# Kernel tuning notes

Measured on AMD Instinct MI355X. Metric: run time of the kernel, lower is better.

Reference implementation:

```python
import jax, jax.numpy as jnp
import numpy as np

NUM_HEADS = 8
CUTOFF = 10.0


def layer_norm(x, g, b):
    m = x.mean(-1, keepdims=True)
    v = x.var(-1, keepdims=True)
    return (x - m) * jax.lax.rsqrt(v + 1e-5) * g + b


def mha(h, mask, Wq, Wk, Wv, Wo):
    # masked multi-head self-attention over the edge set; mask: [E,E] bool
    E, D = h.shape
    hd = D // NUM_HEADS
    q = (h @ Wq).reshape(E, NUM_HEADS, hd)
    k = (h @ Wk).reshape(E, NUM_HEADS, hd)
    v = (h @ Wv).reshape(E, NUM_HEADS, hd)
    s = jnp.einsum('ihd,jhd->hij', q, k) / jnp.sqrt(jnp.asarray(hd, h.dtype))
    s = jnp.where(mask[None], s, jnp.asarray(-1e9, h.dtype))
    p = jax.nn.softmax(s, axis=-1)  # [H,E,E]
    out = jnp.einsum('hij,jhd->ihd', p, v).reshape(E, D)
    return out @ Wo, p.mean(0)


def setup_inputs() -> dict:
    D, L, R, E, N, NB = 128, 3, 64, 3072, 1024, 16
    key = jax.random.key(0)
    ks = jax.random.split(key, 32)
    f32 = jnp.float32

    def w(i, shape, scale):
        return (jax.random.normal(ks[i], shape) * scale).astype(f32)

    s = 1.0 / np.sqrt(D)
    return {
        'edge_features': w(0, (E, D), 1.0),
        'edge_coords': w(1, (E, 3), 1.0),
        'edge_index': jax.random.randint(ks[2], (2, E), 0, N),
        'node_coords': w(3, (N, 3), 5.0),  # spread so distances span [0, cutoff]
        'block_ids': jax.random.randint(ks[4], (N,), 0, NB),
        'Wq_a': w(5, (L, D, D), s), 'Wk_a': w(6, (L, D, D), s),
        'Wv_a': w(7, (L, D, D), s), 'Wo_a': w(8, (L, D, D), s),
        'Wq_e': w(9, (L, D, D), s), 'Wk_e': w(10, (L, D, D), s),
        'Wv_e': w(11, (L, D, D), s), 'Wo_e': w(12, (L, D, D), s),
        'W1': w(13, (L, D, 4 * D), s), 'b1': jnp.zeros((L, 4 * D), f32),
        'W2': w(14, (L, 4 * D, D), 1.0 / np.sqrt(4 * D)), 'b2': jnp.zeros((L, D), f32),
        'ln1_g': jnp.ones((L, D), f32), 'ln1_b': jnp.zeros((L, D), f32),
        'ln2_g': jnp.ones((L, D), f32), 'ln2_b': jnp.zeros((L, D), f32),
        'ln3_g': jnp.ones((L, D), f32), 'ln3_b': jnp.zeros((L, D), f32),
        'Wrbf': w(15, (L, R, D), 1.0 / np.sqrt(R)),
        'Wc': w(16, (L, D), s), 'bc': jnp.zeros((L,), f32),
    }


def reference(edge_features, edge_coords, edge_index, node_coords, block_ids,
              Wq_a, Wk_a, Wv_a, Wo_a, Wq_e, Wk_e, Wv_e, Wo_e,
              W1, b1, W2, b2, ln1_g, ln1_b, ln2_g, ln2_b, ln3_g, ln3_b,
              Wrbf, Wc, bc):
    E = edge_features.shape[0]
    src, dst = edge_index[0], edge_index[1]
    bs, bd = block_ids[src], block_ids[dst]

    # intra-block mask: both endpoint blocks match between the two edges
    intra = (bs[:, None] == bs[None, :]) & (bd[:, None] == bd[None, :])
    # inter-block mask: edges that share a node but cross blocks
    share = ((src[:, None] == src[None, :]) | (src[:, None] == dst[None, :]) |
             (dst[:, None] == src[None, :]) | (dst[:, None] == dst[None, :]))
    inter = share & ~intra
    eye = jnp.eye(E, dtype=bool)
    intra = intra | eye
    inter = inter | eye

    # radial basis embedding of edge length with cosine cutoff
    R = Wrbf.shape[1]
    d = jnp.linalg.norm(node_coords[dst] - node_coords[src], axis=-1)  # [E]
    centers = jnp.linspace(0.0, CUTOFF, R).astype(edge_features.dtype)
    width = CUTOFF / R
    fc = 0.5 * (jnp.cos(jnp.pi * jnp.clip(d / CUTOFF, 0.0, 1.0)) + 1.0)
    rbf = jnp.exp(-(((d[:, None] - centers[None, :]) / width) ** 2)) * fc[:, None]

    h, x = edge_features, edge_coords
    L = Wq_a.shape[0]
    for l in range(L):
        h = h + rbf @ Wrbf[l]
        a, p_intra = mha(h, intra, Wq_a[l], Wk_a[l], Wv_a[l], Wo_a[l])
        h = layer_norm(h + a, ln1_g[l], ln1_b[l])
        e, _ = mha(h, inter, Wq_e[l], Wk_e[l], Wv_e[l], Wo_e[l])
        h = layer_norm(h + e, ln2_g[l], ln2_b[l])
        f = jax.nn.silu(h @ W1[l] + b1[l]) @ W2[l] + b2[l]
        h = layer_norm(h + f, ln3_g[l], ln3_b[l])
        # equivariant coordinate update (linear combination of equivariant vecs)
        gate = jnp.tanh(h @ Wc[l] + bc[l])[:, None]  # [E,1]
        x = x + gate * (x - p_intra @ x)
    return h, x
```

## Files before the change

kernel.cpp:

```cpp
#include <hip/hip_runtime.h>
#include <hip/hip_bf16.h>

typedef unsigned short u16;
typedef unsigned long long u64;
typedef __attribute__((ext_vector_type(4))) float f32x4;
typedef __attribute__((ext_vector_type(8))) short bf16x8;

#define NE 3072
#define DM 128
#define NH 8
#define HD 16
#define NL 3
#define NR 64
#define FF 512
#define CUT 10.0f
#define CAP 96
#define GRID 192
#define BR 16
#define NCLS 256

#define PK_QKV_A 0
#define PK_WO_A  49152
#define PK_QKV_E 65536
#define PK_WO_E  114688
#define PK_W1    131072
#define PK_W2    196608
#define PK_WRBF  262144
#define PK_LAYER 270336

__device__ __forceinline__ short f2b(float f) {
    union { __hip_bfloat16 b; short s; } u;
    u.b = __float2bfloat16(f);
    return u.s;
}
__device__ __forceinline__ void ast64(u64* p, u64 v) {
    __hip_atomic_store(p, v, __ATOMIC_RELAXED, __HIP_MEMORY_SCOPE_AGENT);
}
__device__ __forceinline__ void astf(float* p, float v) {
    __hip_atomic_store(p, v, __ATOMIC_RELAXED, __HIP_MEMORY_SCOPE_AGENT);
}
__device__ __forceinline__ float bfx(u64 v, int i) {
    return __uint_as_float(((unsigned)(v >> (16 * i)) & 0xFFFFu) << 16);
}

template <int KT, int S>
__device__ __forceinline__ f32x4 tileAb(const short* As, const short* Bt, int l) {
    f32x4 acc = {0.f, 0.f, 0.f, 0.f};
#pragma unroll
    for (int kt = 0; kt < KT; kt++) {
        bf16x8 av = *(const bf16x8*)(As + (l & 15) * S + kt * 32 + 8 * (l >> 4));
        bf16x8 bv = *(const bf16x8*)(Bt + kt * 512 + l * 8);
        acc = __builtin_amdgcn_mfma_f32_16x16x32_bf16(av, bv, acc, 0, 0, 0);
    }
    return acc;
}

__device__ __forceinline__ void gbar(int* cnt, int target) {
    __syncthreads();
    if (threadIdx.x == 0) {
        __hip_atomic_fetch_add(cnt, 1, __ATOMIC_RELEASE, __HIP_MEMORY_SCOPE_AGENT);
        while (__hip_atomic_load(cnt, __ATOMIC_RELAXED, __HIP_MEMORY_SCOPE_AGENT) < target)
            __builtin_amdgcn_s_sleep(2);
        asm volatile("" ::: "memory");
    }
    __syncthreads();
}

struct WSrc { const float* W[11]; };

__global__ __launch_bounds__(256)
void pack_w(WSrc ws, short* __restrict__ dst) {
    int gid = blockIdx.x * 256 + threadIdx.x;
    if (gid >= NL * PK_LAYER) return;
    int layer = gid / PK_LAYER, e = gid % PK_LAYER;
    int kind, off, K, N;
    if (e < 49152)       { kind = e / 16384;            off = e % 16384;      K = 128; N = 128; }
    else if (e < 65536)  { kind = 3;                    off = e - 49152;      K = 128; N = 128; }
    else if (e < 114688) { kind = 4 + (e - 65536) / 16384; off = (e - 65536) % 16384; K = 128; N = 128; }
    else if (e < 131072) { kind = 7;                    off = e - 114688;     K = 128; N = 128; }
    else if (e < 196608) { kind = 8;                    off = e - 131072;     K = 128; N = 512; }
    else if (e < 262144) { kind = 9;                    off = e - 196608;     K = 512; N = 128; }
    else                 { kind = 10;                   off = e - 262144;     K = 64;  N = 128; }
    int i = off & 7, lane = (off >> 3) & 63, ft = off >> 9;
    int KT = K >> 5;
    int kt = ft % KT, nt = ft / KT;
    int n = nt * 16 + (lane & 15);
    int k = kt * 32 + 8 * (lane >> 4) + i;
    const float* W = ws.W[kind] + (size_t)layer * K * N;
    dst[gid] = f2b(W[k * N + n]);
}

__global__ void zero_hist(int* hist, int* barcnt) {
    hist[threadIdx.x] = 0;
    if (threadIdx.x == 0) *barcnt = 0;
}

__global__ __launch_bounds__(256)
void k_meta(const int* __restrict__ eidx, const int* __restrict__ bids,
            int4* __restrict__ meta, int* __restrict__ key, int* __restrict__ hist) {
    int e = blockIdx.x * 256 + threadIdx.x;
    if (e >= NE) return;
    int s = eidx[e], d = eidx[NE + e];
    int bs = bids[s], bd = bids[d];
    meta[e] = make_int4(s, d, bs, bd);
    int kk = bs * 16 + bd;
    key[e] = kk;
    atomicAdd(&hist[kk], 1);
}

__global__ __launch_bounds__(256)
void k_scan(const int* __restrict__ hist, int* __restrict__ cls_start,
            int* __restrict__ fill) {
    __shared__ int sh[NCLS];
    int t = threadIdx.x;
    sh[t] = hist[t];
    __syncthreads();
    for (int off = 1; off < NCLS; off <<= 1) {
        int v = (t >= off) ? sh[t - off] : 0;
        __syncthreads();
        sh[t] += v;
        __syncthreads();
    }
    cls_start[t + 1] = sh[t];
    if (t == 0) cls_start[0] = 0;
    fill[t] = sh[t] - hist[t];
}

__global__ __launch_bounds__(256)
void k_scatter(const int* __restrict__ key, int* __restrict__ fill,
               int* __restrict__ perm) {
    int e = blockIdx.x * 256 + threadIdx.x;
    if (e >= NE) return;
    int pos = atomicAdd(&fill[key[e]], 1);
    perm[pos] = e;
}

__global__ __launch_bounds__(64)
void prep2(const float* __restrict__ ef, const float* __restrict__ ec,
           const float* __restrict__ nc, const int* __restrict__ perm,
           const int4* __restrict__ metaO, int4* __restrict__ meta2,
           float* __restrict__ h, float* __restrict__ xv, float* __restrict__ rbf) {
    int p = blockIdx.x, lane = threadIdx.x;
    int e = perm[p];
    int4 me = metaO[e];
    if (lane == 0) meta2[p] = me;
    h[p * DM + lane]      = ef[e * DM + lane];
    h[p * DM + 64 + lane] = ef[e * DM + 64 + lane];
    if (lane < 4) xv[p * 4 + lane] = (lane < 3) ? ec[e * 3 + lane] : 0.f;
    float dx = nc[me.y * 3 + 0] - nc[me.x * 3 + 0];
    float dy = nc[me.y * 3 + 1] - nc[me.x * 3 + 1];
    float dz = nc[me.y * 3 + 2] - nc[me.x * 3 + 2];
    float dist = sqrtf(dx * dx + dy * dy + dz * dz);
    float t = fminf(fmaxf(dist / CUT, 0.f), 1.f);
    float fc = 0.5f * (cosf(3.14159265358979f * t) + 1.f);
    float width = CUT / NR;
    float center = (CUT * lane) / (NR - 1);
    float u = (dist - center) / width;
    rbf[p * NR + lane] = expf(-u * u) * fc;
}

__global__ __launch_bounds__(64)
void build_lists(const int4* __restrict__ meta2,
                 u16* __restrict__ idx_e, int* __restrict__ cnt_e) {
    __shared__ int ce;
    __shared__ u16 be[CAP];
    int i = blockIdx.x, lane = threadIdx.x;
    if (lane == 0) ce = 0;
    __syncthreads();
    int4 mi = meta2[i];
    for (int j = lane; j < NE; j += 64) {
        int4 mj = meta2[j];
        bool intra_b = (mi.z == mj.z) && (mi.w == mj.w);
        bool share = (mi.x == mj.x) || (mi.x == mj.y) ||
                     (mi.y == mj.x) || (mi.y == mj.y);
        bool oke = (share && !intra_b) || (i == j);
        if (oke) { int p = atomicAdd(&ce, 1); if (p < CAP) be[p] = (u16)j; }
    }
    __syncthreads();
    int ne_ = min(ce, CAP);
    if (lane == 0) cnt_e[i] = ne_;
    for (int p = lane; p < ne_; p += 64) idx_e[i * CAP + p] = be[p];
}

__device__ __forceinline__ void attn_intra(
    const short (&qsb)[BR][136], const u64* __restrict__ kvaL,
    const float* __restrict__ xr, const int4* __restrict__ meta2,
    const int* __restrict__ cls_start,
    short (&ob)[BR][136], float (&pxs)[NH][BR][3],
    int m0, int w, int l)
{
    int rowl = l >> 2, sub = l & 3, row = m0 + rowl;
    const u64* q64 = reinterpret_cast<const u64*>(&qsb[rowl][w * HD]);
    u64 qc[4];
#pragma unroll
    for (int t = 0; t < 4; t++) qc[t] = q64[t];
    int4 mr = meta2[row];
    int c = mr.z * 16 + mr.w;
    int nb0 = cls_start[c], nb1 = cls_start[c + 1];

    float m = -1e30f, li = 0.f;
    float acc[HD + 3];
#pragma unroll
    for (int d = 0; d < HD + 3; d++) acc[d] = 0.f;

    int p2 = nb0 + sub;
    bool have = p2 < nb1;
    int pc = have ? p2 : nb0;
    const u64* kb = kvaL + ((size_t)w * NE + pc) * 8;
    u64 kc[4], vc[4];
#pragma unroll
    for (int t = 0; t < 4; t++) { kc[t] = kb[t]; vc[t] = kb[4 + t]; }
    float x0 = xr[pc * 4], x1 = xr[pc * 4 + 1], x2 = xr[pc * 4 + 2];

    while (have) {
        int pn = p2 + 4;
        bool haveN = pn < nb1;
        int pl = haveN ? pn : nb0;
        const u64* kbn = kvaL + ((size_t)w * NE + pl) * 8;
        u64 nk[4], nv[4];
#pragma unroll
        for (int t = 0; t < 4; t++) { nk[t] = kbn[t]; nv[t] = kbn[4 + t]; }
        float nx0 = xr[pl * 4], nx1 = xr[pl * 4 + 1], nx2 = xr[pl * 4 + 2];

        float s = 0.f;
#pragma unroll
        for (int t = 0; t < 4; t++)
#pragma unroll
            for (int i = 0; i < 4; i++) s += bfx(qc[t], i) * bfx(kc[t], i);
        s *= 0.25f;
        if (s > m) {
            float cr = __expf(m - s);
            m = s; li *= cr;
#pragma unroll
            for (int d = 0; d < HD + 3; d++) acc[d] *= cr;
        }
        float pw = __expf(s - m);
        li += pw;
#pragma unroll
        for (int t = 0; t < 4; t++)
#pragma unroll
            for (int i = 0; i < 4; i++) acc[t * 4 + i] += pw * bfx(vc[t], i);
        acc[HD] += pw * x0; acc[HD + 1] += pw * x1; acc[HD + 2] += pw * x2;

        p2 = pn; have = haveN;
#pragma unroll
        for (int t = 0; t < 4; t++) { kc[t] = nk[t]; vc[t] = nv[t]; }
        x0 = nx0; x1 = nx1; x2 = nx2;
    }

    float mA = fmaxf(m, __shfl_xor(m, 1));
    mA = fmaxf(mA, __shfl_xor(mA, 2));
    float cf = __expf(m - mA);
    li *= cf;
#pragma unroll
    for (int d = 0; d < HD + 3; d++) acc[d] *= cf;
#pragma unroll
    for (int off = 1; off <= 2; off <<= 1) {
        li += __shfl_xor(li, off);
#pragma unroll
        for (int d = 0; d < HD + 3; d++) acc[d] += __shfl_xor(acc[d], off);
    }
    if (sub == 0) {
        float inv = 1.f / li;
#pragma unroll
        for (int d = 0; d < HD; d += 2) {
            unsigned loq = (u16)f2b(acc[d] * inv);
            unsigned hiq = (u16)f2b(acc[d + 1] * inv);
            *reinterpret_cast<unsigned*>(&ob[rowl][w * HD + d]) = loq | (hiq << 16);
        }
        pxs[w][rowl][0] = acc[HD] * inv;
        pxs[w][rowl][1] = acc[HD + 1] * inv;
        pxs[w][rowl][2] = acc[HD + 2] * inv;
    }
}

__device__ __forceinline__ void attn_inter(
    const short (&qsb)[BR][136], const u64* __restrict__ kveL,
    const u16* __restrict__ idx, const int* __restrict__ cnt,
    short (&ob)[BR][136], int m0, int w, int l)
{
    int rowl = l >> 2, sub = l & 3, row = m0 + rowl;
    const u64* q64 = reinterpret_cast<const u64*>(&qsb[rowl][w * HD]);
    u64 qc[4];
#pragma unroll
    for (int t = 0; t < 4; t++) qc[t] = q64[t];
    const u64* kvh = kveL + (size_t)w * NE * 8;
    int n = cnt[row];
    float m = -1e30f, li = 0.f;
    float acc[HD];
#pragma unroll
    for (int d = 0; d < HD; d++) acc[d] = 0.f;

    int p = sub;
    bool have = p < n;
    int jc = have ? (int)idx[row * CAP + p] : 0;
    const u64* kb = kvh + (size_t)jc * 8;
    u64 kc[4], vc[4];
#pragma unroll
    for (int t = 0; t < 4; t++) { kc[t] = kb[t]; vc[t] = kb[4 + t]; }

    while (have) {
        int pn = p + 4;
        bool haveN = pn < n;
        int jn = haveN ? (int)idx[row * CAP + pn] : 0;
        const u64* kbn = kvh + (size_t)jn * 8;
        u64 nk[4], nv[4];
#pragma unroll
        for (int t = 0; t < 4; t++) { nk[t] = kbn[t]; nv[t] = kbn[4 + t]; }

        float s = 0.f;
#pragma unroll
        for (int t = 0; t < 4; t++)
#pragma unroll
            for (int i = 0; i < 4; i++) s += bfx(qc[t], i) * bfx(kc[t], i);
        s *= 0.25f;
        if (s > m) {
            float cr = __expf(m - s);
            m = s; li *= cr;
#pragma unroll
            for (int d = 0; d < HD; d++) acc[d] *= cr;
        }
        float pw = __expf(s - m);
        li += pw;
#pragma unroll
        for (int t = 0; t < 4; t++)
#pragma unroll
            for (int i = 0; i < 4; i++) acc[t * 4 + i] += pw * bfx(vc[t], i);

        p = pn; have = haveN;
#pragma unroll
        for (int t = 0; t < 4; t++) { kc[t] = nk[t]; vc[t] = nv[t]; }
    }

    float mA = fmaxf(m, __shfl_xor(m, 1));
    mA = fmaxf(mA, __shfl_xor(mA, 2));
    float cf = __expf(m - mA);
    li *= cf;
#pragma unroll
    for (int d = 0; d < HD; d++) acc[d] *= cf;
#pragma unroll
    for (int off = 1; off <= 2; off <<= 1) {
        li += __shfl_xor(li, off);
#pragma unroll
        for (int d = 0; d < HD; d++) acc[d] += __shfl_xor(acc[d], off);
    }
    if (sub == 0) {
        float inv = 1.f / li;
#pragma unroll
        for (int d = 0; d < HD; d += 2) {
            unsigned loq = (u16)f2b(acc[d] * inv);
            unsigned hiq = (u16)f2b(acc[d + 1] * inv);
            *reinterpret_cast<unsigned*>(&ob[rowl][w * HD + d]) = loq | (hiq << 16);
        }
    }
}

__device__ __forceinline__ void ln_rows(float (&zs)[BR][132], float (&hF)[BR][132],
                                        short* hB, const float* g, const float* b,
                                        int w, int l) {
#pragma unroll
    for (int rr = 0; rr < 2; rr++) {
        int r = 2 * w + rr;
        float z0 = zs[r][l], z1 = zs[r][64 + l];
        float s = z0 + z1;
#pragma unroll
        for (int off = 32; off; off >>= 1) s += __shfl_xor(s, off);
        float mean = s * (1.f / DM);
        float d0 = z0 - mean, d1 = z1 - mean;
        float vs = d0 * d0 + d1 * d1;
#pragma unroll
        for (int off = 32; off; off >>= 1) vs += __shfl_xor(vs, off);
        float inv = rsqrtf(vs * (1.f / DM) + 1e-5f);
        float h0 = d0 * inv * g[l] + b[l];
        float h1 = d1 * inv * g[64 + l] + b[64 + l];
        hF[r][l] = h0; hF[r][64 + l] = h1;
        hB[r * 136 + l] = f2b(h0);
        hB[r * 136 + 64 + l] = f2b(h1);
    }
}

__global__ __launch_bounds__(512, 2)
void mega_kernel(const float* __restrict__ h_init, const float* __restrict__ rbf_g,
                 const int4* __restrict__ meta2, const int* __restrict__ cls_start,
                 const int* __restrict__ perm,
                 const u16* __restrict__ idx_e, const int* __restrict__ cnt_e,
                 const short* __restrict__ pk,
                 const float* __restrict__ b1g, const float* __restrict__ b2g,
                 const float* __restrict__ ln1g, const float* __restrict__ ln1b,
                 const float* __restrict__ ln2g, const float* __restrict__ ln2b,
                 const float* __restrict__ ln3g, const float* __restrict__ ln3b,
                 const float* __restrict__ Wcg, const float* __restrict__ bcg,
                 short* __restrict__ kva, short* __restrict__ kve,
                 float* __restrict__ xv, int* __restrict__ barcnt,
                 float* __restrict__ outp)
{
    __shared__ float hL[BR][132];
    __shared__ float hn[BR][132];
    __shared__ float zs[BR][132];
    __shared__ short qsb[BR][136];
    __shared__ short hb[BR][136];
    __shared__ short hnb[BR][136];
    __shared__ short ob[BR][136];
    __shared__ short rbfb[BR][72];
    __shared__ short ub[BR][520];
    __shared__ float pxs[NH][BR][3];

    int tid = threadIdx.x, w = tid >> 6, l = tid & 63;
    int m0 = blockIdx.x * BR;
    int R4 = 4 * (l >> 4), c0 = l & 15;

    for (int i = tid; i < BR * 128; i += 512) hL[i >> 7][i & 127] = h_init[m0 * DM + i];
    for (int i = tid; i < BR * 64; i += 512) rbfb[i >> 6][i & 63] = f2b(rbf_g[m0 * NR + i]);
    __syncthreads();

    int ph = 0;
    for (int lay = 0; lay < NL; lay++) {
        const short* Lb = pk + (size_t)lay * PK_LAYER;
        const float* xr = xv + (size_t)lay * NE * 4;
        float* xw2 = xv + (size_t)(lay + 1) * NE * 4;
        u64* kvaL = reinterpret_cast<u64*>(kva) + (size_t)lay * NH * NE * 8;
        u64* kveL = reinterpret_cast<u64*>(kve) + (size_t)lay * NH * NE * 8;
        bool last = (lay == NL - 1);

        {
            f32x4 acc = tileAb<2, 72>(&rbfb[0][0], Lb + PK_WRBF + w * 1024, l);
#pragma unroll
            for (int r = 0; r < 4; r++) {
                float z = acc[r] + hL[R4 + r][w * 16 + c0];
                hn[R4 + r][w * 16 + c0] = z;
                hnb[R4 + r][w * 16 + c0] = f2b(z);
            }
        }
        __syncthreads();
        {
            f32x4 aq = tileAb<4, 136>(&hnb[0][0], Lb + PK_QKV_A + 0 * 16384 + w * 2048, l);
#pragma unroll
            for (int r = 0; r < 4; r++) qsb[R4 + r][w * 16 + c0] = f2b(aq[r]);
            f32x4 ak = tileAb<4, 136>(&hnb[0][0], Lb + PK_QKV_A + 1 * 16384 + w * 2048, l);
            f32x4 av = tileAb<4, 136>(&hnb[0][0], Lb + PK_QKV_A + 2 * 16384 + w * 2048, l);
#pragma unroll
            for (int r = 0; r < 4; r++) {
                ub[R4 + r][w * 16 + c0] = f2b(ak[r]);
                ub[R4 + r][128 + w * 16 + c0] = f2b(av[r]);
            }
            __syncthreads();
            for (int u = tid; u < BR * 64; u += 512) {
                int r = u >> 6, rest = u & 63, hh = rest >> 3, j = rest & 7;
                int so = (j < 4) ? (hh * 16 + j * 4) : (128 + hh * 16 + (j - 4) * 4);
                u64 val = *reinterpret_cast<const u64*>(&ub[r][so]);
                ast64(kvaL + ((size_t)hh * NE + m0 + r) * 8 + j, val);
            }
        }
        gbar(barcnt, GRID * (++ph));

        attn_intra(qsb, kvaL, xr, meta2, cls_start, ob, pxs, m0, w, l);
        __syncthreads();
        {
            f32x4 d = tileAb<4, 136>(&ob[0][0], Lb + PK_WO_A + w * 2048, l);
#pragma unroll
            for (int r = 0; r < 4; r++)
                zs[R4 + r][w * 16 + c0] = d[r] + hn[R4 + r][w * 16 + c0];
        }
        __syncthreads();
        ln_rows(zs, hL, &hb[0][0], ln1g + lay * DM, ln1b + lay * DM, w, l);
        __syncthreads();

        {
            f32x4 aq = tileAb<4, 136>(&hb[0][0], Lb + PK_QKV_E + 0 * 16384 + w * 2048, l);
#pragma unroll
            for (int r = 0; r < 4; r++) qsb[R4 + r][w * 16 + c0] = f2b(aq[r]);
            f32x4 ak = tileAb<4, 136>(&hb[0][0], Lb + PK_QKV_E + 1 * 16384 + w * 2048, l);
            f32x4 av = tileAb<4, 136>(&hb[0][0], Lb + PK_QKV_E + 2 * 16384 + w * 2048, l);
#pragma unroll
            for (int r = 0; r < 4; r++) {
                ub[R4 + r][w * 16 + c0] = f2b(ak[r]);
                ub[R4 + r][128 + w * 16 + c0] = f2b(av[r]);
            }
            __syncthreads();
            for (int u = tid; u < BR * 64; u += 512) {
                int r = u >> 6, rest = u & 63, hh = rest >> 3, j = rest & 7;
                int so = (j < 4) ? (hh * 16 + j * 4) : (128 + hh * 16 + (j - 4) * 4);
                u64 val = *reinterpret_cast<const u64*>(&ub[r][so]);
                ast64(kveL + ((size_t)hh * NE + m0 + r) * 8 + j, val);
            }
        }
        gbar(barcnt, GRID * (++ph));

        attn_inter(qsb, kveL, idx_e, cnt_e, ob, m0, w, l);
        __syncthreads();
        {
            f32x4 d = tileAb<4, 136>(&ob[0][0], Lb + PK_WO_E + w * 2048, l);
#pragma unroll
            for (int r = 0; r < 4; r++)
                zs[R4 + r][w * 16 + c0] = d[r] + hL[R4 + r][w * 16 + c0];
        }
        __syncthreads();
        ln_rows(zs, hL, &hb[0][0], ln2g + lay * DM, ln2b + lay * DM, w, l);
        __syncthreads();

#pragma unroll
        for (int j = 0; j < 4; j++) {
            int nt = w * 4 + j;
            f32x4 acc = tileAb<4, 136>(&hb[0][0], Lb + PK_W1 + nt * 2048, l);
#pragma unroll
            for (int r = 0; r < 4; r++) {
                int col = nt * 16 + c0;
                float xvv = acc[r] + b1g[lay * FF + col];
                xvv = xvv / (1.f + __expf(-xvv));
                ub[R4 + r][col] = f2b(xvv);
            }
        }
        __syncthreads();
        {
            f32x4 acc = tileAb<16, 520>(&ub[0][0], Lb + PK_W2 + w * 8192, l);
#pragma unroll
            for (int r = 0; r < 4; r++)
                zs[R4 + r][w * 16 + c0] = acc[r] + b2g[lay * DM + w * 16 + c0]
                                        + hL[R4 + r][w * 16 + c0];
        }
        __syncthreads();
        {
            const float* g3 = ln3g + lay * DM;
            const float* b3 = ln3b + lay * DM;
            const float* Wcl = Wcg + lay * DM;
            float bc0 = bcg[lay];
#pragma unroll
            for (int rr = 0; rr < 2; rr++) {
                int r = 2 * w + rr, row = m0 + r;
                int orow = perm[row];
                float z0 = zs[r][l], z1 = zs[r][64 + l];
                float s = z0 + z1;
#pragma unroll
                for (int off = 32; off; off >>= 1) s += __shfl_xor(s, off);
                float mean = s * (1.f / DM);
                float d0 = z0 - mean, d1 = z1 - mean;
                float vsum = d0 * d0 + d1 * d1;
#pragma unroll
                for (int off = 32; off; off >>= 1) vsum += __shfl_xor(vsum, off);
                float inv = rsqrtf(vsum * (1.f / DM) + 1e-5f);
                float h0 = d0 * inv * g3[l] + b3[l];
                float h1 = d1 * inv * g3[64 + l] + b3[64 + l];
                hL[r][l] = h0; hL[r][64 + l] = h1;
                if (last) { outp[orow * DM + l] = h0; outp[orow * DM + 64 + l] = h1; }
                float dc = h0 * Wcl[l] + h1 * Wcl[64 + l];
#pragma unroll
                for (int off = 32; off; off >>= 1) dc += __shfl_xor(dc, off);
                float gate = tanhf(dc + bc0);
                if (l < 3) {
                    float pxm = 0.f;
#pragma unroll
                    for (int hh = 0; hh < NH; hh++) pxm += pxs[hh][r][l];
                    pxm *= 0.125f;
                    float xvv = xr[row * 4 + l];
                    float nx = xvv + gate * (xvv - pxm);
                    astf(xw2 + row * 4 + l, nx);
                    if (last) outp[NE * DM + orow * 3 + l] = nx;
                }
            }
        }
        __syncthreads();
    }
}

extern "C" void kernel_launch(void* const* d_in, const int* in_sizes, int n_in,
                              void* d_out, int out_size, void* d_ws, size_t ws_size,
                              hipStream_t stream) {
    const float* ef   = (const float*)d_in[0];
    const float* ec   = (const float*)d_in[1];
    const int*   eidx = (const int*)d_in[2];
    const float* nc   = (const float*)d_in[3];
    const int*   bids = (const int*)d_in[4];
    const float* b1   = (const float*)d_in[14];
    const float* b2   = (const float*)d_in[16];
    const float* ln1g = (const float*)d_in[17];
    const float* ln1b = (const float*)d_in[18];
    const float* ln2g = (const float*)d_in[19];
    const float* ln2b = (const float*)d_in[20];
    const float* ln3g = (const float*)d_in[21];
    const float* ln3b = (const float*)d_in[22];
    const float* Wc   = (const float*)d_in[24];
    const float* bc   = (const float*)d_in[25];
    float* out = (float*)d_out;

    char* w = (char*)d_ws;
    auto carve = [&](size_t bytes) { char* p = w; w += ((bytes + 255) / 256) * 256; return p; };
    int*   barcnt = (int*)carve(256);
    int*   hist   = (int*)carve(NCLS * 4);
    int*   csta   = (int*)carve((NCLS + 1) * 4);
    int*   fill   = (int*)carve(NCLS * 4);
    int*   key    = (int*)carve((size_t)NE * 4);
    int*   perm   = (int*)carve((size_t)NE * 4);
    int4*  metaO  = (int4*)carve((size_t)NE * 16);
    int4*  meta2  = (int4*)carve((size_t)NE * 16);
    float* xv     = (float*)carve((size_t)(NL + 1) * NE * 4 * 4);
    int*   cnt_e  = (int*)carve((size_t)NE * 4);
    u16*   idx_e  = (u16*)carve((size_t)NE * CAP * 2);
    float* rbf_g  = (float*)carve((size_t)NE * NR * 4);
    float* h_in   = (float*)carve((size_t)NE * DM * 4);
    short* kva    = (short*)carve((size_t)NL * NH * NE * 32 * 2);
    short* kve    = (short*)carve((size_t)NL * NH * NE * 32 * 2);
    short* pk     = (short*)carve((size_t)NL * PK_LAYER * 2);

    WSrc ws;
    ws.W[0] = (const float*)d_in[5];   ws.W[1] = (const float*)d_in[6];
    ws.W[2] = (const float*)d_in[7];   ws.W[3] = (const float*)d_in[8];
    ws.W[4] = (const float*)d_in[9];   ws.W[5] = (const float*)d_in[10];
    ws.W[6] = (const float*)d_in[11];  ws.W[7] = (const float*)d_in[12];
    ws.W[8] = (const float*)d_in[13];  ws.W[9] = (const float*)d_in[15];
    ws.W[10] = (const float*)d_in[23];
    pack_w<<<(NL * PK_LAYER + 255) / 256, 256, 0, stream>>>(ws, pk);

    zero_hist<<<1, 256, 0, stream>>>(hist, barcnt);
    k_meta<<<(NE + 255) / 256, 256, 0, stream>>>(eidx, bids, metaO, key, hist);
    k_scan<<<1, 256, 0, stream>>>(hist, csta, fill);
    k_scatter<<<(NE + 255) / 256, 256, 0, stream>>>(key, fill, perm);
    prep2<<<NE, 64, 0, stream>>>(ef, ec, nc, perm, metaO, meta2, h_in, xv, rbf_g);
    build_lists<<<NE, 64, 0, stream>>>(meta2, idx_e, cnt_e);

    mega_kernel<<<GRID, 512, 0, stream>>>(h_in, rbf_g, meta2, csta, perm,
                                          idx_e, cnt_e, pk,
                                          b1, b2, ln1g, ln1b, ln2g, ln2b, ln3g, ln3b,
                                          Wc, bc, kva, kve, xv, barcnt, out);
}
```

Baseline: 160.8 us.

## Replace intra-attention grid barrier with per-block flags and fuse prep kernels

```diff
diff --git a/kernel.cpp b/kernel.cpp
--- a/kernel.cpp
+++ b/kernel.cpp
@@ -68,44 +68,42 @@
 
 struct WSrc { const float* W[11]; };
 
+__global__ void zeroK(int* hist, int* barcnt, int* flags) {
+    int t = threadIdx.x;
+    if (t < NCLS) hist[t] = 0;
+    if (t < GRID) flags[t] = 0;
+    if (t == 500) *barcnt = 0;
+}
+
 __global__ __launch_bounds__(256)
-void pack_w(WSrc ws, short* __restrict__ dst) {
+void pack_meta(WSrc ws, short* __restrict__ pkd,
+               const int* __restrict__ eidx, const int* __restrict__ bids,
+               int* __restrict__ key, int* __restrict__ hist) {
     int gid = blockIdx.x * 256 + threadIdx.x;
-    if (gid >= NL * PK_LAYER) return;
-    int layer = gid / PK_LAYER, e = gid % PK_LAYER;
-    int kind, off, K, N;
-    if (e < 49152)       { kind = e / 16384;            off = e % 16384;      K = 128; N = 128; }
-    else if (e < 65536)  { kind = 3;                    off = e - 49152;      K = 128; N = 128; }
-    else if (e < 114688) { kind = 4 + (e - 65536) / 16384; off = (e - 65536) % 16384; K = 128; N = 128; }
-    else if (e < 131072) { kind = 7;                    off = e - 114688;     K = 128; N = 128; }
-    else if (e < 196608) { kind = 8;                    off = e - 131072;     K = 128; N = 512; }
-    else if (e < 262144) { kind = 9;                    off = e - 196608;     K = 512; N = 128; }
-    else                 { kind = 10;                   off = e - 262144;     K = 64;  N = 128; }
-    int i = off & 7, lane = (off >> 3) & 63, ft = off >> 9;
-    int KT = K >> 5;
-    int kt = ft % KT, nt = ft / KT;
-    int n = nt * 16 + (lane & 15);
-    int k = kt * 32 + 8 * (lane >> 4) + i;
-    const float* W = ws.W[kind] + (size_t)layer * K * N;
-    dst[gid] = f2b(W[k * N + n]);
-}
-
-__global__ void zero_hist(int* hist, int* barcnt) {
-    hist[threadIdx.x] = 0;
-    if (threadIdx.x == 0) *barcnt = 0;
-}
-
-__global__ __launch_bounds__(256)
-void k_meta(const int* __restrict__ eidx, const int* __restrict__ bids,
-            int4* __restrict__ meta, int* __restrict__ key, int* __restrict__ hist) {
-    int e = blockIdx.x * 256 + threadIdx.x;
-    if (e >= NE) return;
-    int s = eidx[e], d = eidx[NE + e];
-    int bs = bids[s], bd = bids[d];
-    meta[e] = make_int4(s, d, bs, bd);
-    int kk = bs * 16 + bd;
-    key[e] = kk;
-    atomicAdd(&hist[kk], 1);
+    if (gid < NE) {
+        int s = eidx[gid], d = eidx[NE + gid];
+        int kk = bids[s] * 16 + bids[d];
+        key[gid] = kk;
+        atomicAdd(&hist[kk], 1);
+    }
+    if (gid < NL * PK_LAYER) {
+        int layer = gid / PK_LAYER, e = gid % PK_LAYER;
+        int kind, off, K, N;
+        if (e < 49152)       { kind = e / 16384;            off = e % 16384;      K = 128; N = 128; }
+        else if (e < 65536)  { kind = 3;                    off = e - 49152;      K = 128; N = 128; }
+        else if (e < 114688) { kind = 4 + (e - 65536) / 16384; off = (e - 65536) % 16384; K = 128; N = 128; }
+        else if (e < 131072) { kind = 7;                    off = e - 114688;     K = 128; N = 128; }
+        else if (e < 196608) { kind = 8;                    off = e - 131072;     K = 128; N = 512; }
+        else if (e < 262144) { kind = 9;                    off = e - 196608;     K = 512; N = 128; }
+        else                 { kind = 10;                   off = e - 262144;     K = 64;  N = 128; }
+        int i = off & 7, lane = (off >> 3) & 63, ft = off >> 9;
+        int KT = K >> 5;
+        int kt = ft % KT, nt = ft / KT;
+        int n = nt * 16 + (lane & 15);
+        int k = kt * 32 + 8 * (lane >> 4) + i;
+        const float* W = ws.W[kind] + (size_t)layer * K * N;
+        pkd[gid] = f2b(W[k * N + n]);
+    }
 }
 
 __global__ __launch_bounds__(256)
@@ -127,59 +125,61 @@
 }
 
 __global__ __launch_bounds__(256)
-void k_scatter(const int* __restrict__ key, int* __restrict__ fill,
-               int* __restrict__ perm) {
+void k_scatter(const int* __restrict__ eidx, const int* __restrict__ bids,
+               const int* __restrict__ key, int* __restrict__ fill,
+               int* __restrict__ perm, int4* __restrict__ meta2) {
     int e = blockIdx.x * 256 + threadIdx.x;
     if (e >= NE) return;
     int pos = atomicAdd(&fill[key[e]], 1);
     perm[pos] = e;
-}
-
-__global__ __launch_bounds__(64)
-void prep2(const float* __restrict__ ef, const float* __restrict__ ec,
-           const float* __restrict__ nc, const int* __restrict__ perm,
-           const int4* __restrict__ metaO, int4* __restrict__ meta2,
-           float* __restrict__ h, float* __restrict__ xv, float* __restrict__ rbf) {
-    int p = blockIdx.x, lane = threadIdx.x;
-    int e = perm[p];
-    int4 me = metaO[e];
-    if (lane == 0) meta2[p] = me;
-    h[p * DM + lane]      = ef[e * DM + lane];
-    h[p * DM + 64 + lane] = ef[e * DM + 64 + lane];
-    if (lane < 4) xv[p * 4 + lane] = (lane < 3) ? ec[e * 3 + lane] : 0.f;
-    float dx = nc[me.y * 3 + 0] - nc[me.x * 3 + 0];
-    float dy = nc[me.y * 3 + 1] - nc[me.x * 3 + 1];
-    float dz = nc[me.y * 3 + 2] - nc[me.x * 3 + 2];
-    float dist = sqrtf(dx * dx + dy * dy + dz * dz);
-    float t = fminf(fmaxf(dist / CUT, 0.f), 1.f);
-    float fc = 0.5f * (cosf(3.14159265358979f * t) + 1.f);
-    float width = CUT / NR;
-    float center = (CUT * lane) / (NR - 1);
-    float u = (dist - center) / width;
-    rbf[p * NR + lane] = expf(-u * u) * fc;
-}
-
-__global__ __launch_bounds__(64)
-void build_lists(const int4* __restrict__ meta2,
-                 u16* __restrict__ idx_e, int* __restrict__ cnt_e) {
+    int s = eidx[e], d = eidx[NE + e];
+    meta2[pos] = make_int4(s, d, bids[s], bids[d]);
+}
+
+__global__ __launch_bounds__(128)
+void prep_lists(const float* __restrict__ ef, const float* __restrict__ ec,
+                const float* __restrict__ nc, const int* __restrict__ perm,
+                const int4* __restrict__ meta2,
+                float* __restrict__ h, float* __restrict__ xv, float* __restrict__ rbf,
+                u16* __restrict__ idx_e, int* __restrict__ cnt_e) {
     __shared__ int ce;
     __shared__ u16 be[CAP];
-    int i = blockIdx.x, lane = threadIdx.x;
-    if (lane == 0) ce = 0;
-    __syncthreads();
-    int4 mi = meta2[i];
-    for (int j = lane; j < NE; j += 64) {
-        int4 mj = meta2[j];
-        bool intra_b = (mi.z == mj.z) && (mi.w == mj.w);
-        bool share = (mi.x == mj.x) || (mi.x == mj.y) ||
-                     (mi.y == mj.x) || (mi.y == mj.y);
-        bool oke = (share && !intra_b) || (i == j);
-        if (oke) { int p = atomicAdd(&ce, 1); if (p < CAP) be[p] = (u16)j; }
-    }
-    __syncthreads();
-    int ne_ = min(ce, CAP);
-    if (lane == 0) cnt_e[i] = ne_;
-    for (int p = lane; p < ne_; p += 64) idx_e[i * CAP + p] = be[p];
+    int p = blockIdx.x, t = threadIdx.x;
+    if (t < 64) {
+        int lane = t;
+        int e = perm[p];
+        int4 me = meta2[p];
+        h[p * DM + lane]      = ef[e * DM + lane];
+        h[p * DM + 64 + lane] = ef[e * DM + 64 + lane];
+        if (lane < 4) xv[p * 4 + lane] = (lane < 3) ? ec[e * 3 + lane] : 0.f;
+        float dx = nc[me.y * 3 + 0] - nc[me.x * 3 + 0];
+        float dy = nc[me.y * 3 + 1] - nc[me.x * 3 + 1];
+        float dz = nc[me.y * 3 + 2] - nc[me.x * 3 + 2];
+        float dist = sqrtf(dx * dx + dy * dy + dz * dz);
+        float tt = fminf(fmaxf(dist / CUT, 0.f), 1.f);
+        float fc = 0.5f * (cosf(3.14159265358979f * tt) + 1.f);
+        float width = CUT / NR;
+        float center = (CUT * lane) / (NR - 1);
+        float u = (dist - center) / width;
+        rbf[p * NR + lane] = expf(-u * u) * fc;
+    } else {
+        int lane = t - 64;
+        if (lane == 0) ce = 0;
+        __builtin_amdgcn_wave_barrier();
+        int4 mi = meta2[p];
+        for (int j = lane; j < NE; j += 64) {
+            int4 mj = meta2[j];
+            bool intra_b = (mi.z == mj.z) && (mi.w == mj.w);
+            bool share = (mi.x == mj.x) || (mi.x == mj.y) ||
+                         (mi.y == mj.x) || (mi.y == mj.y);
+            bool oke = (share && !intra_b) || (p == j);
+            if (oke) { int q = atomicAdd(&ce, 1); if (q < CAP) be[q] = (u16)j; }
+        }
+        __builtin_amdgcn_wave_barrier();
+        int ne_ = min(ce, CAP);
+        if (lane == 0) cnt_e[p] = ne_;
+        for (int q = lane; q < ne_; q += 64) idx_e[p * CAP + q] = be[q];
+    }
 }
 
 __device__ __forceinline__ void attn_intra(
@@ -392,7 +392,7 @@
                  const float* __restrict__ Wcg, const float* __restrict__ bcg,
                  short* __restrict__ kva, short* __restrict__ kve,
                  float* __restrict__ xv, int* __restrict__ barcnt,
-                 float* __restrict__ outp)
+                 int* __restrict__ flags, float* __restrict__ outp)
 {
     __shared__ float hL[BR][132];
     __shared__ float hn[BR][132];
@@ -409,11 +409,15 @@
     int m0 = blockIdx.x * BR;
     int R4 = 4 * (l >> 4), c0 = l & 15;
 
+    int4 mFirst = meta2[m0], mLast = meta2[m0 + BR - 1];
+    int spanLo = cls_start[mFirst.z * 16 + mFirst.w];
+    int spanHi = cls_start[mLast.z * 16 + mLast.w + 1];
+    int sb0 = spanLo >> 4, sb1 = (spanHi - 1) >> 4;
+
     for (int i = tid; i < BR * 128; i += 512) hL[i >> 7][i & 127] = h_init[m0 * DM + i];
     for (int i = tid; i < BR * 64; i += 512) rbfb[i >> 6][i & 63] = f2b(rbf_g[m0 * NR + i]);
     __syncthreads();
 
-    int ph = 0;
     for (int lay = 0; lay < NL; lay++) {
         const short* Lb = pk + (size_t)lay * PK_LAYER;
         const float* xr = xv + (size_t)lay * NE * 4;
@@ -451,7 +455,17 @@
                 ast64(kvaL + ((size_t)hh * NE + m0 + r) * 8 + j, val);
             }
         }
-        gbar(barcnt, GRID * (++ph));
+        __syncthreads();
+        if (tid == 0) {
+            __hip_atomic_store(flags + blockIdx.x, lay + 1, __ATOMIC_RELEASE,
+                               __HIP_MEMORY_SCOPE_AGENT);
+            for (int b = sb0; b <= sb1; b++)
+                while (__hip_atomic_load(flags + b, __ATOMIC_RELAXED,
+                                         __HIP_MEMORY_SCOPE_AGENT) < lay + 1)
+                    __builtin_amdgcn_s_sleep(1);
+            asm volatile("" ::: "memory");
+        }
+        __syncthreads();
 
         attn_intra(qsb, kvaL, xr, meta2, cls_start, ob, pxs, m0, w, l);
         __syncthreads();
@@ -484,7 +498,7 @@
                 ast64(kveL + ((size_t)hh * NE + m0 + r) * 8 + j, val);
             }
         }
-        gbar(barcnt, GRID * (++ph));
+        gbar(barcnt, GRID * (lay + 1));
 
         attn_inter(qsb, kveL, idx_e, cnt_e, ob, m0, w, l);
         __syncthreads();
@@ -585,12 +599,12 @@
     char* w = (char*)d_ws;
     auto carve = [&](size_t bytes) { char* p = w; w += ((bytes + 255) / 256) * 256; return p; };
     int*   barcnt = (int*)carve(256);
+    int*   flags  = (int*)carve(GRID * 4);
     int*   hist   = (int*)carve(NCLS * 4);
     int*   csta   = (int*)carve((NCLS + 1) * 4);
     int*   fill   = (int*)carve(NCLS * 4);
     int*   key    = (int*)carve((size_t)NE * 4);
     int*   perm   = (int*)carve((size_t)NE * 4);
-    int4*  metaO  = (int4*)carve((size_t)NE * 16);
     int4*  meta2  = (int4*)carve((size_t)NE * 16);
     float* xv     = (float*)carve((size_t)(NL + 1) * NE * 4 * 4);
     int*   cnt_e  = (int*)carve((size_t)NE * 4);
@@ -608,17 +622,15 @@
     ws.W[6] = (const float*)d_in[11];  ws.W[7] = (const float*)d_in[12];
     ws.W[8] = (const float*)d_in[13];  ws.W[9] = (const float*)d_in[15];
     ws.W[10] = (const float*)d_in[23];
-    pack_w<<<(NL * PK_LAYER + 255) / 256, 256, 0, stream>>>(ws, pk);
-
-    zero_hist<<<1, 256, 0, stream>>>(hist, barcnt);
-    k_meta<<<(NE + 255) / 256, 256, 0, stream>>>(eidx, bids, metaO, key, hist);
+
+    zeroK<<<1, 512, 0, stream>>>(hist, barcnt, flags);
+    pack_meta<<<(NL * PK_LAYER + 255) / 256, 256, 0, stream>>>(ws, pk, eidx, bids, key, hist);
     k_scan<<<1, 256, 0, stream>>>(hist, csta, fill);
-    k_scatter<<<(NE + 255) / 256, 256, 0, stream>>>(key, fill, perm);
-    prep2<<<NE, 64, 0, stream>>>(ef, ec, nc, perm, metaO, meta2, h_in, xv, rbf_g);
-    build_lists<<<NE, 64, 0, stream>>>(meta2, idx_e, cnt_e);
+    k_scatter<<<(NE + 255) / 256, 256, 0, stream>>>(eidx, bids, key, fill, perm, meta2);
+    prep_lists<<<NE, 128, 0, stream>>>(ef, ec, nc, perm, meta2, h_in, xv, rbf_g, idx_e, cnt_e);
 
     mega_kernel<<<GRID, 512, 0, stream>>>(h_in, rbf_g, meta2, csta, perm,
                                           idx_e, cnt_e, pk,
                                           b1, b2, ln1g, ln1b, ln2g, ln2b, ln3g, ln3b,
-                                          Wc, bc, kva, kve, xv, barcnt, out);
-}
+                                          Wc, bc, kva, kve, xv, barcnt, flags, out);
+}
```

Result: slower. 171.7 us (+6.8%).

## Use 1024-thread blocks with 32 rows each and half the persistent grid

Applied to the files above, without the earlier changes.

```diff
diff --git a/kernel.cpp b/kernel.cpp
--- a/kernel.cpp
+++ b/kernel.cpp
@@ -15,8 +15,9 @@
 #define FF 512
 #define CUT 10.0f
 #define CAP 96
-#define GRID 192
-#define BR 16
+#define GRID 96
+#define BR 32
+#define THREADS 1024
 #define NCLS 256
 
 #define PK_QKV_A 0
@@ -187,10 +188,11 @@
     const float* __restrict__ xr, const int4* __restrict__ meta2,
     const int* __restrict__ cls_start,
     short (&ob)[BR][136], float (&pxs)[NH][BR][3],
-    int m0, int w, int l)
+    int m0, int tid)
 {
-    int rowl = l >> 2, sub = l & 3, row = m0 + rowl;
-    const u64* q64 = reinterpret_cast<const u64*>(&qsb[rowl][w * HD]);
+    int unit = tid >> 2, sub = tid & 3;
+    int rowl = unit >> 3, head = unit & 7, row = m0 + rowl;
+    const u64* q64 = reinterpret_cast<const u64*>(&qsb[rowl][head * HD]);
     u64 qc[4];
 #pragma unroll
     for (int t = 0; t < 4; t++) qc[t] = q64[t];
@@ -206,7 +208,7 @@
     int p2 = nb0 + sub;
     bool have = p2 < nb1;
     int pc = have ? p2 : nb0;
-    const u64* kb = kvaL + ((size_t)w * NE + pc) * 8;
+    const u64* kb = kvaL + ((size_t)head * NE + pc) * 8;
     u64 kc[4], vc[4];
 #pragma unroll
     for (int t = 0; t < 4; t++) { kc[t] = kb[t]; vc[t] = kb[4 + t]; }
@@ -216,7 +218,7 @@
         int pn = p2 + 4;
         bool haveN = pn < nb1;
         int pl = haveN ? pn : nb0;
-        const u64* kbn = kvaL + ((size_t)w * NE + pl) * 8;
+        const u64* kbn = kvaL + ((size_t)head * NE + pl) * 8;
         u64 nk[4], nv[4];
 #pragma unroll
         for (int t = 0; t < 4; t++) { nk[t] = kbn[t]; nv[t] = kbn[4 + t]; }
@@ -266,25 +268,26 @@
         for (int d = 0; d < HD; d += 2) {
             unsigned loq = (u16)f2b(acc[d] * inv);
             unsigned hiq = (u16)f2b(acc[d + 1] * inv);
-            *reinterpret_cast<unsigned*>(&ob[rowl][w * HD + d]) = loq | (hiq << 16);
-        }
-        pxs[w][rowl][0] = acc[HD] * inv;
-        pxs[w][rowl][1] = acc[HD + 1] * inv;
-        pxs[w][rowl][2] = acc[HD + 2] * inv;
+            *reinterpret_cast<unsigned*>(&ob[rowl][head * HD + d]) = loq | (hiq << 16);
+        }
+        pxs[head][rowl][0] = acc[HD] * inv;
+        pxs[head][rowl][1] = acc[HD + 1] * inv;
+        pxs[head][rowl][2] = acc[HD + 2] * inv;
     }
 }
 
 __device__ __forceinline__ void attn_inter(
     const short (&qsb)[BR][136], const u64* __restrict__ kveL,
     const u16* __restrict__ idx, const int* __restrict__ cnt,
-    short (&ob)[BR][136], int m0, int w, int l)
+    short (&ob)[BR][136], int m0, int tid)
 {
-    int rowl = l >> 2, sub = l & 3, row = m0 + rowl;
-    const u64* q64 = reinterpret_cast<const u64*>(&qsb[rowl][w * HD]);
+    int unit = tid >> 2, sub = tid & 3;
+    int rowl = unit >> 3, head = unit & 7, row = m0 + rowl;
+    const u64* q64 = reinterpret_cast<const u64*>(&qsb[rowl][head * HD]);
     u64 qc[4];
 #pragma unroll
     for (int t = 0; t < 4; t++) qc[t] = q64[t];
-    const u64* kvh = kveL + (size_t)w * NE * 8;
+    const u64* kvh = kveL + (size_t)head * NE * 8;
     int n = cnt[row];
     float m = -1e30f, li = 0.f;
     float acc[HD];
@@ -350,7 +353,7 @@
         for (int d = 0; d < HD; d += 2) {
             unsigned loq = (u16)f2b(acc[d] * inv);
             unsigned hiq = (u16)f2b(acc[d + 1] * inv);
-            *reinterpret_cast<unsigned*>(&ob[rowl][w * HD + d]) = loq | (hiq << 16);
+            *reinterpret_cast<unsigned*>(&ob[rowl][head * HD + d]) = loq | (hiq << 16);
         }
     }
 }
@@ -379,7 +382,7 @@
     }
 }
 
-__global__ __launch_bounds__(512, 2)
+__global__ __launch_bounds__(THREADS)
 void mega_kernel(const float* __restrict__ h_init, const float* __restrict__ rbf_g,
                  const int4* __restrict__ meta2, const int* __restrict__ cls_start,
                  const int* __restrict__ perm,
@@ -408,9 +411,11 @@
     int tid = threadIdx.x, w = tid >> 6, l = tid & 63;
     int m0 = blockIdx.x * BR;
     int R4 = 4 * (l >> 4), c0 = l & 15;
-
-    for (int i = tid; i < BR * 128; i += 512) hL[i >> 7][i & 127] = h_init[m0 * DM + i];
-    for (int i = tid; i < BR * 64; i += 512) rbfb[i >> 6][i & 63] = f2b(rbf_g[m0 * NR + i]);
+    int rt = w >> 3, ct = w & 7;
+    int rb = rt * 16;
+
+    for (int i = tid; i < BR * 128; i += THREADS) hL[i >> 7][i & 127] = h_init[m0 * DM + i];
+    for (int i = tid; i < BR * 64; i += THREADS) rbfb[i >> 6][i & 63] = f2b(rbf_g[m0 * NR + i]);
     __syncthreads();
 
     int ph = 0;
@@ -423,28 +428,28 @@
         bool last = (lay == NL - 1);
 
         {
-            f32x4 acc = tileAb<2, 72>(&rbfb[0][0], Lb + PK_WRBF + w * 1024, l);
+            f32x4 acc = tileAb<2, 72>(&rbfb[rb][0], Lb + PK_WRBF + ct * 1024, l);
 #pragma unroll
             for (int r = 0; r < 4; r++) {
-                float z = acc[r] + hL[R4 + r][w * 16 + c0];
-                hn[R4 + r][w * 16 + c0] = z;
-                hnb[R4 + r][w * 16 + c0] = f2b(z);
+                float z = acc[r] + hL[rb + R4 + r][ct * 16 + c0];
+                hn[rb + R4 + r][ct * 16 + c0] = z;
+                hnb[rb + R4 + r][ct * 16 + c0] = f2b(z);
             }
         }
         __syncthreads();
         {
-            f32x4 aq = tileAb<4, 136>(&hnb[0][0], Lb + PK_QKV_A + 0 * 16384 + w * 2048, l);
-#pragma unroll
-            for (int r = 0; r < 4; r++) qsb[R4 + r][w * 16 + c0] = f2b(aq[r]);
-            f32x4 ak = tileAb<4, 136>(&hnb[0][0], Lb + PK_QKV_A + 1 * 16384 + w * 2048, l);
-            f32x4 av = tileAb<4, 136>(&hnb[0][0], Lb + PK_QKV_A + 2 * 16384 + w * 2048, l);
+            f32x4 aq = tileAb<4, 136>(&hnb[rb][0], Lb + PK_QKV_A + 0 * 16384 + ct * 2048, l);
+#pragma unroll
+            for (int r = 0; r < 4; r++) qsb[rb + R4 + r][ct * 16 + c0] = f2b(aq[r]);
+            f32x4 ak = tileAb<4, 136>(&hnb[rb][0], Lb + PK_QKV_A + 1 * 16384 + ct * 2048, l);
+            f32x4 av = tileAb<4, 136>(&hnb[rb][0], Lb + PK_QKV_A + 2 * 16384 + ct * 2048, l);
 #pragma unroll
             for (int r = 0; r < 4; r++) {
-                ub[R4 + r][w * 16 + c0] = f2b(ak[r]);
-                ub[R4 + r][128 + w * 16 + c0] = f2b(av[r]);
+                ub[rb + R4 + r][ct * 16 + c0] = f2b(ak[r]);
+                ub[rb + R4 + r][128 + ct * 16 + c0] = f2b(av[r]);
             }
             __syncthreads();
-            for (int u = tid; u < BR * 64; u += 512) {
+            for (int u = tid; u < BR * 64; u += THREADS) {
                 int r = u >> 6, rest = u & 63, hh = rest >> 3, j = rest & 7;
                 int so = (j < 4) ? (hh * 16 + j * 4) : (128 + hh * 16 + (j - 4) * 4);
                 u64 val = *reinterpret_cast<const u64*>(&ub[r][so]);
@@ -453,31 +458,31 @@
         }
         gbar(barcnt, GRID * (++ph));
 
-        attn_intra(qsb, kvaL, xr, meta2, cls_start, ob, pxs, m0, w, l);
+        attn_intra(qsb, kvaL, xr, meta2, cls_start, ob, pxs, m0, tid);
         __syncthreads();
         {
-            f32x4 d = tileAb<4, 136>(&ob[0][0], Lb + PK_WO_A + w * 2048, l);
+            f32x4 d = tileAb<4, 136>(&ob[rb][0], Lb + PK_WO_A + ct * 2048, l);
 #pragma unroll
             for (int r = 0; r < 4; r++)
-                zs[R4 + r][w * 16 + c0] = d[r] + hn[R4 + r][w * 16 + c0];
+                zs[rb + R4 + r][ct * 16 + c0] = d[r] + hn[rb + R4 + r][ct * 16 + c0];
         }
         __syncthreads();
         ln_rows(zs, hL, &hb[0][0], ln1g + lay * DM, ln1b + lay * DM, w, l);
         __syncthreads();
 
         {
-            f32x4 aq = tileAb<4, 136>(&hb[0][0], Lb + PK_QKV_E + 0 * 16384 + w * 2048, l);
-#pragma unroll
-            for (int r = 0; r < 4; r++) qsb[R4 + r][w * 16 + c0] = f2b(aq[r]);
-            f32x4 ak = tileAb<4, 136>(&hb[0][0], Lb + PK_QKV_E + 1 * 16384 + w * 2048, l);
-            f32x4 av = tileAb<4, 136>(&hb[0][0], Lb + PK_QKV_E + 2 * 16384 + w * 2048, l);
+            f32x4 aq = tileAb<4, 136>(&hb[rb][0], Lb + PK_QKV_E + 0 * 16384 + ct * 2048, l);
+#pragma unroll
+            for (int r = 0; r < 4; r++) qsb[rb + R4 + r][ct * 16 + c0] = f2b(aq[r]);
+            f32x4 ak = tileAb<4, 136>(&hb[rb][0], Lb + PK_QKV_E + 1 * 16384 + ct * 2048, l);
+            f32x4 av = tileAb<4, 136>(&hb[rb][0], Lb + PK_QKV_E + 2 * 16384 + ct * 2048, l);
 #pragma unroll
             for (int r = 0; r < 4; r++) {
-                ub[R4 + r][w * 16 + c0] = f2b(ak[r]);
-                ub[R4 + r][128 + w * 16 + c0] = f2b(av[r]);
+                ub[rb + R4 + r][ct * 16 + c0] = f2b(ak[r]);
+                ub[rb + R4 + r][128 + ct * 16 + c0] = f2b(av[r]);
             }
             __syncthreads();
-            for (int u = tid; u < BR * 64; u += 512) {
+            for (int u = tid; u < BR * 64; u += THREADS) {
                 int r = u >> 6, rest = u & 63, hh = rest >> 3, j = rest & 7;
                 int so = (j < 4) ? (hh * 16 + j * 4) : (128 + hh * 16 + (j - 4) * 4);
                 u64 val = *reinterpret_cast<const u64*>(&ub[r][so]);
@@ -486,13 +491,13 @@
         }
         gbar(barcnt, GRID * (++ph));
 
-        attn_inter(qsb, kveL, idx_e, cnt_e, ob, m0, w, l);
+        attn_inter(qsb, kveL, idx_e, cnt_e, ob, m0, tid);
         __syncthreads();
         {
-            f32x4 d = tileAb<4, 136>(&ob[0][0], Lb + PK_WO_E + w * 2048, l);
+            f32x4 d = tileAb<4, 136>(&ob[rb][0], Lb + PK_WO_E + ct * 2048, l);
 #pragma unroll
             for (int r = 0; r < 4; r++)
-                zs[R4 + r][w * 16 + c0] = d[r] + hL[R4 + r][w * 16 + c0];
+                zs[rb + R4 + r][ct * 16 + c0] = d[r] + hL[rb + R4 + r][ct * 16 + c0];
         }
         __syncthreads();
         ln_rows(zs, hL, &hb[0][0], ln2g + lay * DM, ln2b + lay * DM, w, l);
@@ -500,23 +505,24 @@
 
 #pragma unroll
         for (int j = 0; j < 4; j++) {
-            int nt = w * 4 + j;
-            f32x4 acc = tileAb<4, 136>(&hb[0][0], Lb + PK_W1 + nt * 2048, l);
+            int t = w * 4 + j;
+            int rtt = t >> 5, ctt = t & 31;
+            f32x4 acc = tileAb<4, 136>(&hb[rtt * 16][0], Lb + PK_W1 + ctt * 2048, l);
 #pragma unroll
             for (int r = 0; r < 4; r++) {
-                int col = nt * 16 + c0;
+                int col = ctt * 16 + c0;
                 float xvv = acc[r] + b1g[lay * FF + col];
                 xvv = xvv / (1.f + __expf(-xvv));
-                ub[R4 + r][col] = f2b(xvv);
+                ub[rtt * 16 + R4 + r][col] = f2b(xvv);
             }
         }
         __syncthreads();
         {
-            f32x4 acc = tileAb<16, 520>(&ub[0][0], Lb + PK_W2 + w * 8192, l);
+            f32x4 acc = tileAb<16, 520>(&ub[rb][0], Lb + PK_W2 + ct * 8192, l);
 #pragma unroll
             for (int r = 0; r < 4; r++)
-                zs[R4 + r][w * 16 + c0] = acc[r] + b2g[lay * DM + w * 16 + c0]
-                                        + hL[R4 + r][w * 16 + c0];
+                zs[rb + R4 + r][ct * 16 + c0] = acc[r] + b2g[lay * DM + ct * 16 + c0]
+                                              + hL[rb + R4 + r][ct * 16 + c0];
         }
         __syncthreads();
         {
@@ -617,8 +623,8 @@
     prep2<<<NE, 64, 0, stream>>>(ef, ec, nc, perm, metaO, meta2, h_in, xv, rbf_g);
     build_lists<<<NE, 64, 0, stream>>>(meta2, idx_e, cnt_e);
 
-    mega_kernel<<<GRID, 512, 0, stream>>>(h_in, rbf_g, meta2, csta, perm,
-                                          idx_e, cnt_e, pk,
-                                          b1, b2, ln1g, ln1b, ln2g, ln2b, ln3g, ln3b,
-                                          Wc, bc, kva, kve, xv, barcnt, out);
-}
+    mega_kernel<<<GRID, THREADS, 0, stream>>>(h_in, rbf_g, meta2, csta, perm,
+                                              idx_e, cnt_e, pk,
+                                              b1, b2, ln1g, ln1b, ln2g, ln2b, ln3g, ln3b,
+                                              Wc, bc, kva, kve, xv, barcnt, out);
+}
```

After: 199.8 us. +24.3%, slower.
